# Optimization experiments

Hardware: AMD Instinct MI355X
Metric: run time of the kernel (lower is better)

## Reference

```python
import jax, jax.numpy as jnp
import numpy as np

B, N, D, H = 2, 2048, 1024, 16
DH = D // H
DF = 4 * D
SCALE = D ** (-0.5)  # standard_scale=False -> dim**-0.5
EPS = 1e-5


def _ln(x, w, b):
    mu = jnp.mean(x, axis=-1, keepdims=True)
    var = jnp.mean(jnp.square(x - mu), axis=-1, keepdims=True)
    return (x - mu) * jax.lax.rsqrt(var + EPS) * w + b


def setup_inputs() -> dict:
    key = jax.random.key(0)
    ks = jax.random.split(key, 12)
    s = lambda fan_in: (1.0 / np.sqrt(fan_in))
    return {
        "x": jax.random.normal(ks[0], (B, N, D), jnp.float32),
        "gamma": jax.random.uniform(ks[1], (B, H), jnp.float32),
        "dist_matrix": jax.random.uniform(ks[2], (N, N), jnp.float32),
        "ln1_w": jnp.ones((D,), jnp.float32),
        "ln1_b": jnp.zeros((D,), jnp.float32),
        "qkv_w": jax.random.normal(ks[3], (D, 3 * D), jnp.float32) * s(D),
        "qkv_b": jnp.zeros((3 * D,), jnp.float32),
        "proj_w": jax.random.normal(ks[4], (D, D), jnp.float32) * s(D),
        "proj_b": jnp.zeros((D,), jnp.float32),
        "ln2_w": jnp.ones((D,), jnp.float32),
        "ln2_b": jnp.zeros((D,), jnp.float32),
        "mlp_w1": jax.random.normal(ks[5], (D, DF), jnp.float32) * s(D),
        "mlp_b1": jnp.zeros((DF,), jnp.float32),
        "mlp_w2": jax.random.normal(ks[6], (DF, D), jnp.float32) * s(DF),
        "mlp_b2": jnp.zeros((D,), jnp.float32),
    }


def reference(x, gamma, dist_matrix, ln1_w, ln1_b, qkv_w, qkv_b, proj_w, proj_b,
              ln2_w, ln2_b, mlp_w1, mlp_b1, mlp_w2, mlp_b2):
    # --- ZoomAttention on norm1(x) ---
    h = _ln(x, ln1_w, ln1_b)                                   # [B,N,D]
    qkv = h @ qkv_w + qkv_b                                    # [B,N,3D]
    qkv = qkv.reshape(B, N, 3, H, DH).transpose(2, 0, 3, 1, 4)  # [3,B,H,N,DH]
    q, k, v = qkv[0], qkv[1], qkv[2]
    scores = jnp.einsum("bhnd,bhmd->bhnm", q, k) * SCALE       # [B,H,N,N]
    scores = scores - gamma[:, :, None, None] * dist_matrix[None, None]
    attn = jax.nn.softmax(scores, axis=-1)
    out = jnp.einsum("bhnm,bhmd->bhnd", attn, v)               # [B,H,N,DH]
    out = out.transpose(0, 2, 1, 3).reshape(B, N, D)
    x = x + (out @ proj_w + proj_b)
    # --- MLP (exact GELU, torch default) ---
    h2 = _ln(x, ln2_w, ln2_b)
    h2 = jax.nn.gelu(h2 @ mlp_w1 + mlp_b1, approximate=False) @ mlp_w2 + mlp_b2
    return x + h2
```

## Files before the change

### kernel.cpp

```cpp
#include <hip/hip_runtime.h>
#include <hip/hip_bf16.h>


#define SCALE_ 0.03125f
#define EPS_   1e-5f
#define LOG2E_ 1.4426950408889634f
#define SC2_   (SCALE_ * LOG2E_)

typedef unsigned short u16;
typedef __attribute__((ext_vector_type(8))) short short8;
typedef __attribute__((ext_vector_type(4))) float f32x4;
typedef __attribute__((ext_vector_type(4))) unsigned short u16x4;

__device__ inline float b2f(u16 u){ unsigned x = ((unsigned)u) << 16; float f; __builtin_memcpy(&f, &x, 4); return f; }
__device__ inline u16 f2b(float f){ __hip_bfloat16 h = __float2bfloat16(f); u16 u; __builtin_memcpy(&u, &h, 2); return u; }

__device__ inline void glds16(const u16* g, u16* l) {
    __builtin_amdgcn_global_load_lds(
        (const __attribute__((address_space(1))) void*)g,
        (__attribute__((address_space(3))) void*)l, 16, 0, 0);
}

__device__ inline unsigned cvtpk(float a, float b) {
    unsigned r;
    asm("v_cvt_pk_bf16_f32 %0, %1, %2" : "=v"(r) : "v"(a), "v"(b));
    return r;
}

__global__ __launch_bounds__(256) void prep_fused(
    const float* __restrict__ s0, const float* __restrict__ s1,
    const float* __restrict__ s2, const float* __restrict__ s3,
    u16* __restrict__ d0, u16* __restrict__ d1,
    u16* __restrict__ d2, u16* __restrict__ d3,
    const float* __restrict__ x, const float* __restrict__ lw,
    const float* __restrict__ lb, u16* __restrict__ ho) {
    int bid = blockIdx.x;
    if (bid < 12288) {
        __shared__ float t[32][33];
        const float* src; u16* dst; int K, N, nbx, base;
        if (bid < 3072)      { src = s0; dst = d0; K = 1024; N = 3072; nbx = 96;  base = 0; }
        else if (bid < 4096) { src = s1; dst = d1; K = 1024; N = 1024; nbx = 32;  base = 3072; }
        else if (bid < 8192) { src = s2; dst = d2; K = 1024; N = 4096; nbx = 128; base = 4096; }
        else                 { src = s3; dst = d3; K = 4096; N = 1024; nbx = 32;  base = 8192; }
        int lb2 = bid - base;
        int nb = (lb2 % nbx) * 32, kb = (lb2 / nbx) * 32;
        int tx = threadIdx.x & 31, ty = threadIdx.x >> 5;
        for (int i = 0; i < 4; i++) {
            int r = ty + i * 8;
            t[r][tx] = src[(size_t)(kb + r) * N + nb + tx];
        }
        __syncthreads();
        for (int i = 0; i < 4; i++) {
            int r = ty + i * 8;
            dst[(size_t)(nb + r) * K + kb + tx] = f2b(t[tx][r]);
        }
    } else {
        int row = bid - 12288, t = threadIdx.x;
        float4 v = ((const float4*)(x + (size_t)row * 1024))[t];
        float s1v = v.x + v.y + v.z + v.w;
        float s2v = v.x * v.x + v.y * v.y + v.z * v.z + v.w * v.w;
        for (int o = 32; o > 0; o >>= 1) { s1v += __shfl_xor(s1v, o); s2v += __shfl_xor(s2v, o); }
        __shared__ float a1[4], a2[4];
        if ((t & 63) == 0) { a1[t >> 6] = s1v; a2[t >> 6] = s2v; }
        __syncthreads();
        s1v = a1[0] + a1[1] + a1[2] + a1[3];
        s2v = a2[0] + a2[1] + a2[2] + a2[3];
        float mu = s1v * (1.0f / 1024.0f);
        float var = s2v * (1.0f / 1024.0f) - mu * mu;
        float rs = rsqrtf(var + EPS_);
        float4 wv = ((const float4*)lw)[t];
        float4 bv = ((const float4*)lb)[t];
        u16x4 o;
        o[0] = f2b((v.x - mu) * rs * wv.x + bv.x);
        o[1] = f2b((v.y - mu) * rs * wv.y + bv.y);
        o[2] = f2b((v.z - mu) * rs * wv.z + bv.z);
        o[3] = f2b((v.w - mu) * rs * wv.w + bv.w);
        ((u16x4*)(ho + (size_t)row * 1024))[t] = o;
    }
}

__global__ __launch_bounds__(256) void ln_bf16(const float* __restrict__ x,
                                               const float* __restrict__ w,
                                               const float* __restrict__ b,
                                               u16* __restrict__ out) {
    int row = blockIdx.x, t = threadIdx.x;
    float4 v = ((const float4*)(x + (size_t)row * 1024))[t];
    float s1 = v.x + v.y + v.z + v.w;
    float s2 = v.x * v.x + v.y * v.y + v.z * v.z + v.w * v.w;
    for (int o = 32; o > 0; o >>= 1) { s1 += __shfl_xor(s1, o); s2 += __shfl_xor(s2, o); }
    __shared__ float a1[4], a2[4];
    if ((t & 63) == 0) { a1[t >> 6] = s1; a2[t >> 6] = s2; }
    __syncthreads();
    s1 = a1[0] + a1[1] + a1[2] + a1[3];
    s2 = a2[0] + a2[1] + a2[2] + a2[3];
    float mu = s1 * (1.0f / 1024.0f);
    float var = s2 * (1.0f / 1024.0f) - mu * mu;
    float rs = rsqrtf(var + EPS_);
    float4 wv = ((const float4*)w)[t];
    float4 bv = ((const float4*)b)[t];
    u16x4 o;
    o[0] = f2b((v.x - mu) * rs * wv.x + bv.x);
    o[1] = f2b((v.y - mu) * rs * wv.y + bv.y);
    o[2] = f2b((v.z - mu) * rs * wv.z + bv.z);
    o[3] = f2b((v.w - mu) * rs * wv.w + bv.w);
    ((u16x4*)(out + (size_t)row * 1024))[t] = o;
}

__global__ __launch_bounds__(256) void combine4(
    const u16* __restrict__ p0, const u16* __restrict__ p1,
    const u16* __restrict__ p2, const u16* __restrict__ p3,
    const float* __restrict__ bias, float* __restrict__ out) {
    size_t i = (size_t)(blockIdx.x * 256 + threadIdx.x) * 4;
    u16x4 a0 = *(const u16x4*)(p0 + i);
    u16x4 a1 = *(const u16x4*)(p1 + i);
    u16x4 a2 = *(const u16x4*)(p2 + i);
    u16x4 a3 = *(const u16x4*)(p3 + i);
    float4 ov = *(float4*)(out + i);
    float4 bv = *(const float4*)(bias + (i & 1023));
    ov.x += b2f(a0[0]) + b2f(a1[0]) + b2f(a2[0]) + b2f(a3[0]) + bv.x;
    ov.y += b2f(a0[1]) + b2f(a1[1]) + b2f(a2[1]) + b2f(a3[1]) + bv.y;
    ov.z += b2f(a0[2]) + b2f(a1[2]) + b2f(a2[2]) + b2f(a3[2]) + bv.z;
    ov.w += b2f(a0[3]) + b2f(a1[3]) + b2f(a2[3]) + b2f(a3[3]) + bv.w;
    *(float4*)(out + i) = ov;
}

template <int MODE>
__global__ __launch_bounds__(512) void gemm256_8ph(
    const u16* __restrict__ A, const u16* __restrict__ Bt,
    const float* __restrict__ bias, int K, int ksl,
    u16* __restrict__ outb,
    u16* __restrict__ qp, u16* __restrict__ kp, u16* __restrict__ vtp) {
    __shared__ u16 LS[4][2][256 * 32];
    int tid = threadIdx.x;
    int w = tid >> 6, lane = tid & 63, g = lane >> 4, ln = lane & 15;
    int wr = w >> 2, wc = w & 3;
    int gx = gridDim.x;
    int nwg = gx * gridDim.y;
    int lin = blockIdx.y * gx + blockIdx.x;
    int swz = (lin & 7) * (nwg >> 3) + (lin >> 3);
    int bx = swz % gx, by = swz / gx;
    int br = by * 256, bc = bx * 256;
    int k0 = blockIdx.z * ksl;
    int jx = (((lane & 3) ^ ((lane >> 3) & 3)) << 3);
    const u16* Ast = A + (size_t)(br + w * 32 + (lane >> 2)) * K + k0 + jx;
    const u16* Bst = Bt + (size_t)(bc + w * 32 + (lane >> 2)) * K + k0 + jx;
    size_t r16 = (size_t)16 * K;
    const int ldsW = (w * 32) * 32;
    f32x4 acc[8][4] = {};
    int NT = ksl >> 5;
    int slotr = ((g ^ ((ln >> 1) & 3)) << 3);
    for (int kt = 0; kt < 3; ++kt) {
        glds16(Ast + (size_t)kt * 32, &LS[kt][0][ldsW]);
        glds16(Ast + (size_t)kt * 32 + r16, &LS[kt][0][ldsW + 512]);
        glds16(Bst + (size_t)kt * 32, &LS[kt][1][ldsW]);
        glds16(Bst + (size_t)kt * 32 + r16, &LS[kt][1][ldsW + 512]);
    }
    asm volatile("s_waitcnt vmcnt(8)" ::: "memory");
    __builtin_amdgcn_s_barrier();
    short8 aa[4], bb[4];
    for (int kt = 0; kt < NT; ++kt) {
        const u16* bufA = &LS[kt & 3][0][0];
        const u16* bufB = &LS[kt & 3][1][0];
        int s3 = kt + 3;
        #pragma unroll
        for (int m = 0; m < 4; ++m)
            aa[m] = *(const short8*)&bufA[(wr * 128 + m * 16 + ln) * 32 + slotr];
        #pragma unroll
        for (int n = 0; n < 4; ++n)
            bb[n] = *(const short8*)&bufB[(wc * 64 + n * 16 + ln) * 32 + slotr];
        if (s3 < NT) {
            u16* d = &LS[s3 & 3][0][ldsW];
            glds16(Ast + (size_t)s3 * 32, d);
            glds16(Ast + (size_t)s3 * 32 + r16, d + 512);
        }
        __builtin_amdgcn_s_barrier();
        asm volatile("s_waitcnt lgkmcnt(0)" ::: "memory");
        __builtin_amdgcn_sched_barrier(0);
        __builtin_amdgcn_s_setprio(1);
        #pragma unroll
        for (int m = 0; m < 4; ++m)
            #pragma unroll
            for (int n = 0; n < 4; ++n)
                acc[m][n] = __builtin_amdgcn_mfma_f32_16x16x32_bf16(aa[m], bb[n], acc[m][n], 0, 0, 0);
        __builtin_amdgcn_s_setprio(0);
        __builtin_amdgcn_sched_barrier(0);
        __builtin_amdgcn_s_barrier();
        #pragma unroll
        for (int m = 0; m < 4; ++m)
            aa[m] = *(const short8*)&bufA[(wr * 128 + 64 + m * 16 + ln) * 32 + slotr];
        if (s3 < NT) {
            u16* d = &LS[s3 & 3][1][ldsW];
            glds16(Bst + (size_t)s3 * 32, d);
            glds16(Bst + (size_t)s3 * 32 + r16, d + 512);
        }
        if (kt + 3 < NT)      asm volatile("s_waitcnt vmcnt(8)" ::: "memory");
        else if (kt + 2 < NT) asm volatile("s_waitcnt vmcnt(4)" ::: "memory");
        else if (kt + 1 < NT) asm volatile("s_waitcnt vmcnt(0)" ::: "memory");
        __builtin_amdgcn_s_barrier();
        asm volatile("s_waitcnt lgkmcnt(0)" ::: "memory");
        __builtin_amdgcn_sched_barrier(0);
        __builtin_amdgcn_s_setprio(1);
        #pragma unroll
        for (int m = 0; m < 4; ++m)
            #pragma unroll
            for (int n = 0; n < 4; ++n)
                acc[4 + m][n] = __builtin_amdgcn_mfma_f32_16x16x32_bf16(aa[m], bb[n], acc[4 + m][n], 0, 0, 0);
        __builtin_amdgcn_s_setprio(0);
        __builtin_amdgcn_sched_barrier(0);
        __builtin_amdgcn_s_barrier();
    }
    #pragma unroll
    for (int m = 0; m < 8; ++m) {
        int row0 = br + wr * 128 + m * 16 + g * 4;
        #pragma unroll
        for (int n = 0; n < 4; ++n) {
            int col = bc + wc * 64 + n * 16 + ln;
            if constexpr (MODE == 0) {
                float bv = bias[col];
                int which = col >> 10, cc = col & 1023, hh = cc >> 6, dh = cc & 63;
                int bb2 = row0 >> 11, nn0 = row0 & 2047;
                size_t bh = (size_t)(bb2 * 16 + hh);
                if (which == 0) {
                    for (int r = 0; r < 4; r++)
                        qp[((bh * 2048 + nn0 + r) << 6) + dh] = f2b((acc[m][n][r] + bv) * SC2_);
                } else if (which == 1) {
                    for (int r = 0; r < 4; r++)
                        kp[((bh * 2048 + nn0 + r) << 6) + dh] = f2b(acc[m][n][r] + bv);
                } else {
                    u16x4 o;
                    for (int r = 0; r < 4; r++) o[r] = f2b(acc[m][n][r] + bv);
                    *(u16x4*)&vtp[((bh * 64 + dh) << 11) + nn0] = o;
                }
            } else if constexpr (MODE == 2) {
                float bv = bias[col];
                for (int r = 0; r < 4; r++) {
                    float v = acc[m][n][r] + bv;
                    float gl = 0.5f * v * (1.0f + erff(v * 0.7071067811865476f));
                    outb[(size_t)(row0 + r) * 4096 + col] = f2b(gl);
                }
            } else {
                u16* pb = (blockIdx.z == 0) ? outb : (blockIdx.z == 1) ? qp
                        : (blockIdx.z == 2) ? kp : vtp;
                for (int r = 0; r < 4; r++)
                    pb[(size_t)(row0 + r) * 1024 + col] = f2b(acc[m][n][r]);
            }
        }
    }
}

template <int MODE, int BN>
__global__ __launch_bounds__(256) void gemm_bf16(
    const u16* __restrict__ A, const u16* __restrict__ Bt,
    const float* __restrict__ bias, int M, int N, int K,
    const float* __restrict__ res, float* __restrict__ outf) {
    constexpr int NN = BN / 32;
    __shared__ u16 As[128 * 64];
    __shared__ u16 Bs[BN * 64];
    int br = blockIdx.y * 128, bc = blockIdx.x * BN;
    int tid = threadIdx.x;
    int w = tid >> 6, lane = tid & 63, g = lane >> 4, ln = lane & 15;
    int wr = (w >> 1) * 64, wc = (w & 1) * (BN / 2);
    f32x4 acc[4][NN] = {};
    int sgcol = (((lane & 7) ^ (lane >> 3)) << 3);
    int arow = w * 32 + (lane >> 3);
    int brow = w * (BN / 4) + (lane >> 3);
    const u16* Ap = A + (size_t)(br + arow) * K + sgcol;
    const u16* Bp = Bt + (size_t)(bc + brow) * K + sgcol;
    u16* lA = &As[(w * 32) * 64];
    u16* lB = &Bs[(w * (BN / 4)) * 64];
    size_t rstep = (size_t)8 * K;
    for (int kt = 0; kt < K; kt += 64) {
        __syncthreads();
        #pragma unroll
        for (int i = 0; i < 4; i++) glds16(Ap + kt + i * rstep, lA + i * 512);
        #pragma unroll
        for (int i = 0; i < BN / 32; i++) glds16(Bp + kt + i * rstep, lB + i * 512);
        __syncthreads();
        #pragma unroll
        for (int kk = 0; kk < 2; kk++) {
            int so = (((kk << 2) + g) ^ (ln & 7)) << 3;
            short8 af[4], bfr[NN];
            #pragma unroll
            for (int m = 0; m < 4; m++)  af[m]  = *(const short8*)&As[(wr + m * 16 + ln) * 64 + so];
            #pragma unroll
            for (int n = 0; n < NN; n++) bfr[n] = *(const short8*)&Bs[(wc + n * 16 + ln) * 64 + so];
            #pragma unroll
            for (int m = 0; m < 4; m++)
                #pragma unroll
                for (int n = 0; n < NN; n++)
                    acc[m][n] = __builtin_amdgcn_mfma_f32_16x16x32_bf16(af[m], bfr[n], acc[m][n], 0, 0, 0);
        }
    }
    #pragma unroll
    for (int m = 0; m < 4; m++) {
        int row0 = br + wr + m * 16 + g * 4;
        #pragma unroll
        for (int n = 0; n < NN; n++) {
            int col = bc + wc + n * 16 + ln;
            float bv = bias[col];
            for (int r = 0; r < 4; r++) {
                size_t idx = (size_t)(row0 + r) * 1024 + col;
                outf[idx] = res[idx] + acc[m][n][r] + bv;
            }
        }
    }
}

__global__ __launch_bounds__(512) void attn_fwd(
    const u16* __restrict__ qg, const u16* __restrict__ kg, const u16* __restrict__ vtg,
    const float* __restrict__ dist, const float* __restrict__ gamma, u16* __restrict__ ao) {
    __shared__ u16 Ks[2][64 * 64];
    __shared__ u16 Vs[2][64 * 64];
    __shared__ u16 Ps[8][16 * 64];
    int qt = blockIdx.x, bh = blockIdx.y;
    int b = bh >> 4, h = bh & 15;
    int tid = threadIdx.x, w = tid >> 6, lane = tid & 63, g = lane >> 4, ln = lane & 15;
    float gam = gamma[bh] * LOG2E_;
    int qglob = qt * 128 + w * 16 + ln;
    const u16* qrow = qg + ((size_t)bh * 2048 + qglob) * 64;
    short8 qf0 = *(const short8*)(qrow + g * 8);
    short8 qf1 = *(const short8*)(qrow + 32 + g * 8);
    const float* dbase = dist + (size_t)qglob * 2048 + g * 4;
    float m2 = -3.0e38f, lsum = 0.0f;
    f32x4 acco[4] = {};
    int srow = tid >> 3, seg = tid & 7;
    int ss = ((seg ^ (srow & 7)) << 3);
    const u16* kgp = kg + ((size_t)bh * 2048 + srow) * 64 + seg * 8;
    const u16* vgp = vtg + ((size_t)bh * 64 + srow) * 2048 + seg * 8;
    {
        short8 a0 = *(const short8*)(kgp);
        short8 c0 = *(const short8*)(vgp);
        *(short8*)&Ks[0][srow * 64 + ss] = a0;
        *(short8*)&Vs[0][srow * 64 + ss] = c0;
    }
    f32x4 dcv[4];
    #pragma unroll
    for (int nb = 0; nb < 4; nb++) dcv[nb] = *(const f32x4*)(dbase + nb * 16);
    __syncthreads();
    int cur = 0;
    int so0 = (g ^ (ln & 7)) << 3, so1 = ((4 + g) ^ (ln & 7)) << 3;
    for (int kt = 0; kt < 32; kt++) {
        short8 kr0, vr0;
        f32x4 dnx[4];
        if (kt < 31) {
            kr0 = *(const short8*)(kgp + (kt + 1) * 4096);
            vr0 = *(const short8*)(vgp + (kt + 1) * 64);
            #pragma unroll
            for (int nb = 0; nb < 4; nb++)
                dnx[nb] = *(const f32x4*)(dbase + (kt + 1) * 64 + nb * 16);
        }
        f32x4 sa[4] = {};
        __builtin_amdgcn_s_setprio(1);
        #pragma unroll
        for (int nb = 0; nb < 4; nb++) {
            short8 kf0 = *(const short8*)&Ks[cur][(nb * 16 + ln) * 64 + so0];
            short8 kf1 = *(const short8*)&Ks[cur][(nb * 16 + ln) * 64 + so1];
            sa[nb] = __builtin_amdgcn_mfma_f32_16x16x32_bf16(kf0, qf0, sa[nb], 0, 0, 0);
            sa[nb] = __builtin_amdgcn_mfma_f32_16x16x32_bf16(kf1, qf1, sa[nb], 0, 0, 0);
        }
        __builtin_amdgcn_s_setprio(0);
        float sv[4][4], pm = -3.0e38f;
        #pragma unroll
        for (int nb = 0; nb < 4; nb++) {
            #pragma unroll
            for (int r = 0; r < 4; r++)
                sv[nb][r] = sa[nb][r] - gam * dcv[nb][r];
            pm = fmaxf(pm, fmaxf(fmaxf(sv[nb][0], sv[nb][1]), fmaxf(sv[nb][2], sv[nb][3])));
        }
        pm = fmaxf(pm, __shfl_xor(pm, 16));
        pm = fmaxf(pm, __shfl_xor(pm, 32));
        if (!__all(pm - m2 <= 8.0f)) {
            float nm = fmaxf(m2, pm);
            float al = __builtin_exp2f(m2 - nm);
            m2 = nm;
            lsum *= al;
            #pragma unroll
            for (int db = 0; db < 4; db++) acco[db] *= al;
        }
        #pragma unroll
        for (int nb = 0; nb < 4; nb++) {
            float e0 = __builtin_exp2f(sv[nb][0] - m2);
            float e1 = __builtin_exp2f(sv[nb][1] - m2);
            float e2 = __builtin_exp2f(sv[nb][2] - m2);
            float e3 = __builtin_exp2f(sv[nb][3] - m2);
            lsum += (e0 + e1) + (e2 + e3);
            union { unsigned u[2]; u16x4 v; } pk;
            pk.u[0] = cvtpk(e0, e1);
            pk.u[1] = cvtpk(e2, e3);
            int off = nb * 16 + g * 4;
            *(u16x4*)&Ps[w][ln * 64 + (((off >> 3) ^ (ln & 7)) << 3) + (off & 7)] = pk.v;
        }
        short8 pf0 = *(const short8*)&Ps[w][ln * 64 + so0];
        short8 pf1 = *(const short8*)&Ps[w][ln * 64 + so1];
        __builtin_amdgcn_s_setprio(1);
        #pragma unroll
        for (int db = 0; db < 4; db++) {
            short8 vf0 = *(const short8*)&Vs[cur][(db * 16 + ln) * 64 + so0];
            short8 vf1 = *(const short8*)&Vs[cur][(db * 16 + ln) * 64 + so1];
            acco[db] = __builtin_amdgcn_mfma_f32_16x16x32_bf16(vf0, pf0, acco[db], 0, 0, 0);
            acco[db] = __builtin_amdgcn_mfma_f32_16x16x32_bf16(vf1, pf1, acco[db], 0, 0, 0);
        }
        __builtin_amdgcn_s_setprio(0);
        if (kt < 31) {
            int nx = cur ^ 1;
            *(short8*)&Ks[nx][srow * 64 + ss] = kr0;
            *(short8*)&Vs[nx][srow * 64 + ss] = vr0;
            #pragma unroll
            for (int nb = 0; nb < 4; nb++) dcv[nb] = dnx[nb];
            __syncthreads();
            cur = nx;
        }
    }
    lsum += __shfl_xor(lsum, 16);
    lsum += __shfl_xor(lsum, 32);
    float inv = 1.0f / lsum;
    u16* aop = ao + (size_t)(b * 2048 + qglob) * 1024 + h * 64 + g * 4;
    #pragma unroll
    for (int db = 0; db < 4; db++) {
        u16x4 o;
        #pragma unroll
        for (int r = 0; r < 4; r++) o[r] = f2b(acco[db][r] * inv);
        *(u16x4*)(aop + db * 16) = o;
    }
}

extern "C" void kernel_launch(void* const* d_in, const int* in_sizes, int n_in,
                              void* d_out, int out_size, void* d_ws, size_t ws_size,
                              hipStream_t stream) {
    const float* x     = (const float*)d_in[0];
    const float* gamma = (const float*)d_in[1];
    const float* dist  = (const float*)d_in[2];
    const float* ln1w  = (const float*)d_in[3];
    const float* ln1b  = (const float*)d_in[4];
    const float* qkvw  = (const float*)d_in[5];
    const float* qkvb  = (const float*)d_in[6];
    const float* projw = (const float*)d_in[7];
    const float* projb = (const float*)d_in[8];
    const float* ln2w  = (const float*)d_in[9];
    const float* ln2b  = (const float*)d_in[10];
    const float* w1    = (const float*)d_in[11];
    const float* b1    = (const float*)d_in[12];
    const float* w2    = (const float*)d_in[13];
    const float* b2    = (const float*)d_in[14];
    float* out = (float*)d_out;
    char* ws = (char*)d_ws;
    u16* wqkvT  = (u16*)(ws + 0);
    u16* wprojT = (u16*)(ws + 6291456);
    u16* w1T    = (u16*)(ws + 8388608);
    u16* w2T    = (u16*)(ws + 16777216);
    u16* hb     = (u16*)(ws + 33554432);
    u16* qb     = (u16*)(ws + 41943040);
    u16* kb     = (u16*)(ws + 50331648);
    u16* vtb    = (u16*)(ws + 58720256);
    u16* aob    = (u16*)(ws + 67108864);
    u16* gb     = hb;
    u16* h2b    = aob;
    u16* mp0 = (u16*)(ws + 0);
    u16* mp1 = (u16*)(ws + 8388608);
    u16* mp2 = (u16*)(ws + 25165824);
    u16* mp3 = (u16*)(ws + 67108864);

    dim3 blk(256);
    prep_fused<<<16384, blk, 0, stream>>>(qkvw, projw, w1, w2,
                                          wqkvT, wprojT, w1T, w2T,
                                          x, ln1w, ln1b, hb);
    gemm256_8ph<0><<<dim3(12, 16), dim3(512), 0, stream>>>(hb, wqkvT, qkvb, 1024, 1024,
                                                           nullptr, qb, kb, vtb);
    attn_fwd<<<dim3(16, 32), dim3(512), 0, stream>>>(qb, kb, vtb, dist, gamma, aob);
    gemm_bf16<1, 64><<<dim3(16, 32), blk, 0, stream>>>(aob, wprojT, projb, 4096, 1024, 1024,
                                                       x, out);
    ln_bf16<<<4096, blk, 0, stream>>>(out, ln2w, ln2b, h2b);
    gemm256_8ph<2><<<dim3(16, 16), dim3(512), 0, stream>>>(h2b, w1T, b1, 1024, 1024,
                                                           gb, nullptr, nullptr, nullptr);
    gemm256_8ph<3><<<dim3(4, 16, 4), dim3(512), 0, stream>>>(gb, w2T, nullptr, 4096, 1024,
                                                             mp0, mp1, mp2, mp3);
    combine4<<<4096, blk, 0, stream>>>(mp0, mp1, mp2, mp3, b2, out);
}
```

Before: 254.3 us.

## Split attention over two key halves with a separate log-sum-exp merge kernel

Result: slower. 269.8 us (+6.1%).

```diff
diff --git a/kernel.cpp b/kernel.cpp
--- a/kernel.cpp
+++ b/kernel.cpp
@@ -122,6 +122,32 @@
     ov.z += b2f(a0[2]) + b2f(a1[2]) + b2f(a2[2]) + b2f(a3[2]) + bv.z;
     ov.w += b2f(a0[3]) + b2f(a1[3]) + b2f(a2[3]) + b2f(a3[3]) + bv.w;
     *(float4*)(out + i) = ov;
+}
+
+__global__ __launch_bounds__(256) void attn_merge(
+    const u16* __restrict__ pO0, const u16* __restrict__ pO1,
+    const float2* __restrict__ ml0, const float2* __restrict__ ml1,
+    u16* __restrict__ ao) {
+    int t = blockIdx.x * 256 + threadIdx.x;
+    int bh = t >> 11, q = t & 2047;
+    int b = bh >> 4, h = bh & 15;
+    float2 s0 = ml0[t], s1 = ml1[t];
+    float M = fmaxf(s0.x, s1.x);
+    float e0 = __builtin_exp2f(s0.x - M);
+    float e1 = __builtin_exp2f(s1.x - M);
+    float inv = 1.0f / (e0 * s0.y + e1 * s1.y);
+    float c0 = e0 * inv, c1 = e1 * inv;
+    const u16x4* r0 = (const u16x4*)(pO0 + (size_t)t * 64);
+    const u16x4* r1 = (const u16x4*)(pO1 + (size_t)t * 64);
+    u16* aop = ao + ((size_t)(b * 2048 + q)) * 1024 + h * 64;
+    #pragma unroll
+    for (int i = 0; i < 16; ++i) {
+        u16x4 a = r0[i], c = r1[i], o;
+        #pragma unroll
+        for (int j = 0; j < 4; ++j)
+            o[j] = f2b(b2f(a[j]) * c0 + b2f(c[j]) * c1);
+        *(u16x4*)(aop + i * 4) = o;
+    }
 }
 
 template <int MODE>
@@ -308,25 +334,26 @@
 
 __global__ __launch_bounds__(512) void attn_fwd(
     const u16* __restrict__ qg, const u16* __restrict__ kg, const u16* __restrict__ vtg,
-    const float* __restrict__ dist, const float* __restrict__ gamma, u16* __restrict__ ao) {
+    const float* __restrict__ dist, const float* __restrict__ gamma,
+    u16* __restrict__ pO0, u16* __restrict__ pO1,
+    float2* __restrict__ ml0, float2* __restrict__ ml1) {
     __shared__ u16 Ks[2][64 * 64];
     __shared__ u16 Vs[2][64 * 64];
     __shared__ u16 Ps[8][16 * 64];
-    int qt = blockIdx.x, bh = blockIdx.y;
-    int b = bh >> 4, h = bh & 15;
+    int qt = blockIdx.x, bh = blockIdx.y, z = blockIdx.z;
     int tid = threadIdx.x, w = tid >> 6, lane = tid & 63, g = lane >> 4, ln = lane & 15;
     float gam = gamma[bh] * LOG2E_;
     int qglob = qt * 128 + w * 16 + ln;
     const u16* qrow = qg + ((size_t)bh * 2048 + qglob) * 64;
     short8 qf0 = *(const short8*)(qrow + g * 8);
     short8 qf1 = *(const short8*)(qrow + 32 + g * 8);
-    const float* dbase = dist + (size_t)qglob * 2048 + g * 4;
+    const float* dbase = dist + (size_t)qglob * 2048 + z * 1024 + g * 4;
     float m2 = -3.0e38f, lsum = 0.0f;
     f32x4 acco[4] = {};
     int srow = tid >> 3, seg = tid & 7;
     int ss = ((seg ^ (srow & 7)) << 3);
-    const u16* kgp = kg + ((size_t)bh * 2048 + srow) * 64 + seg * 8;
-    const u16* vgp = vtg + ((size_t)bh * 64 + srow) * 2048 + seg * 8;
+    const u16* kgp = kg + ((size_t)(bh * 2048 + z * 1024 + srow)) * 64 + seg * 8;
+    const u16* vgp = vtg + ((size_t)(bh * 64 + srow)) * 2048 + z * 1024 + seg * 8;
     {
         short8 a0 = *(const short8*)(kgp);
         short8 c0 = *(const short8*)(vgp);
@@ -339,10 +366,10 @@
     __syncthreads();
     int cur = 0;
     int so0 = (g ^ (ln & 7)) << 3, so1 = ((4 + g) ^ (ln & 7)) << 3;
-    for (int kt = 0; kt < 32; kt++) {
+    for (int kt = 0; kt < 16; kt++) {
         short8 kr0, vr0;
         f32x4 dnx[4];
-        if (kt < 31) {
+        if (kt < 15) {
             kr0 = *(const short8*)(kgp + (kt + 1) * 4096);
             vr0 = *(const short8*)(vgp + (kt + 1) * 64);
             #pragma unroll
@@ -401,7 +428,7 @@
             acco[db] = __builtin_amdgcn_mfma_f32_16x16x32_bf16(vf1, pf1, acco[db], 0, 0, 0);
         }
         __builtin_amdgcn_s_setprio(0);
-        if (kt < 31) {
+        if (kt < 15) {
             int nx = cur ^ 1;
             *(short8*)&Ks[nx][srow * 64 + ss] = kr0;
             *(short8*)&Vs[nx][srow * 64 + ss] = vr0;
@@ -413,14 +440,18 @@
     }
     lsum += __shfl_xor(lsum, 16);
     lsum += __shfl_xor(lsum, 32);
-    float inv = 1.0f / lsum;
-    u16* aop = ao + (size_t)(b * 2048 + qglob) * 1024 + h * 64 + g * 4;
+    int rowid = (bh << 11) + qglob;
+    u16* po = (z ? pO1 : pO0) + (size_t)rowid * 64 + g * 4;
     #pragma unroll
     for (int db = 0; db < 4; db++) {
         u16x4 o;
         #pragma unroll
-        for (int r = 0; r < 4; r++) o[r] = f2b(acco[db][r] * inv);
-        *(u16x4*)(aop + db * 16) = o;
+        for (int r = 0; r < 4; r++) o[r] = f2b(acco[db][r]);
+        *(u16x4*)(po + db * 16) = o;
+    }
+    if (g == 0) {
+        float2 s; s.x = m2; s.y = lsum;
+        (z ? ml1 : ml0)[rowid] = s;
     }
 }
 
@@ -455,6 +486,10 @@
     u16* aob    = (u16*)(ws + 67108864);
     u16* gb     = hb;
     u16* h2b    = aob;
+    u16*    pO0 = (u16*)(ws + 25165824);
+    u16*    pO1 = (u16*)(ws + 33554432);
+    float2* ml0 = (float2*)(ws + 0);
+    float2* ml1 = (float2*)(ws + 1048576);
     u16* mp0 = (u16*)(ws + 0);
     u16* mp1 = (u16*)(ws + 8388608);
     u16* mp2 = (u16*)(ws + 25165824);
@@ -466,7 +501,9 @@
                                           x, ln1w, ln1b, hb);
     gemm256_8ph<0><<<dim3(12, 16), dim3(512), 0, stream>>>(hb, wqkvT, qkvb, 1024, 1024,
                                                            nullptr, qb, kb, vtb);
-    attn_fwd<<<dim3(16, 32), dim3(512), 0, stream>>>(qb, kb, vtb, dist, gamma, aob);
+    attn_fwd<<<dim3(16, 32, 2), dim3(512), 0, stream>>>(qb, kb, vtb, dist, gamma,
+                                                        pO0, pO1, ml0, ml1);
+    attn_merge<<<256, blk, 0, stream>>>(pO0, pO1, ml0, ml1, aob);
     gemm_bf16<1, 64><<<dim3(16, 32), blk, 0, stream>>>(aob, wprojT, projb, 4096, 1024, 1024,
                                                        x, out);
     ln_bf16<<<4096, blk, 0, stream>>>(out, ln2w, ln2b, h2b);
```

## Software-pipeline attention: compute next tile's QK scores during current softmax

Applied to the files above, without the earlier changes.

Measured after the change: 271.4 us. +6.7%, slower.

```diff
diff --git a/kernel.cpp b/kernel.cpp
--- a/kernel.cpp
+++ b/kernel.cpp
@@ -309,8 +309,8 @@
 __global__ __launch_bounds__(512) void attn_fwd(
     const u16* __restrict__ qg, const u16* __restrict__ kg, const u16* __restrict__ vtg,
     const float* __restrict__ dist, const float* __restrict__ gamma, u16* __restrict__ ao) {
-    __shared__ u16 Ks[2][64 * 64];
-    __shared__ u16 Vs[2][64 * 64];
+    __shared__ u16 Ks[4][64 * 64];
+    __shared__ u16 Vs[4][64 * 64];
     __shared__ u16 Ps[8][16 * 64];
     int qt = blockIdx.x, bh = blockIdx.y;
     int b = bh >> 4, h = bh & 15;
@@ -330,87 +330,116 @@
     {
         short8 a0 = *(const short8*)(kgp);
         short8 c0 = *(const short8*)(vgp);
+        short8 a1 = *(const short8*)(kgp + 4096);
+        short8 c1 = *(const short8*)(vgp + 64);
         *(short8*)&Ks[0][srow * 64 + ss] = a0;
         *(short8*)&Vs[0][srow * 64 + ss] = c0;
+        *(short8*)&Ks[1][srow * 64 + ss] = a1;
+        *(short8*)&Vs[1][srow * 64 + ss] = c1;
     }
     f32x4 dcv[4];
     #pragma unroll
     for (int nb = 0; nb < 4; nb++) dcv[nb] = *(const f32x4*)(dbase + nb * 16);
     __syncthreads();
-    int cur = 0;
     int so0 = (g ^ (ln & 7)) << 3, so1 = ((4 + g) ^ (ln & 7)) << 3;
-    for (int kt = 0; kt < 32; kt++) {
-        short8 kr0, vr0;
-        f32x4 dnx[4];
-        if (kt < 31) {
-            kr0 = *(const short8*)(kgp + (kt + 1) * 4096);
-            vr0 = *(const short8*)(vgp + (kt + 1) * 64);
-            #pragma unroll
-            for (int nb = 0; nb < 4; nb++)
-                dnx[nb] = *(const f32x4*)(dbase + (kt + 1) * 64 + nb * 16);
-        }
-        f32x4 sa[4] = {};
+    f32x4 saA[4] = {}, saB[4] = {};
+    {
         __builtin_amdgcn_s_setprio(1);
         #pragma unroll
         for (int nb = 0; nb < 4; nb++) {
-            short8 kf0 = *(const short8*)&Ks[cur][(nb * 16 + ln) * 64 + so0];
-            short8 kf1 = *(const short8*)&Ks[cur][(nb * 16 + ln) * 64 + so1];
-            sa[nb] = __builtin_amdgcn_mfma_f32_16x16x32_bf16(kf0, qf0, sa[nb], 0, 0, 0);
-            sa[nb] = __builtin_amdgcn_mfma_f32_16x16x32_bf16(kf1, qf1, sa[nb], 0, 0, 0);
+            short8 kf0 = *(const short8*)&Ks[0][(nb * 16 + ln) * 64 + so0];
+            short8 kf1 = *(const short8*)&Ks[0][(nb * 16 + ln) * 64 + so1];
+            saA[nb] = __builtin_amdgcn_mfma_f32_16x16x32_bf16(kf0, qf0, saA[nb], 0, 0, 0);
+            saA[nb] = __builtin_amdgcn_mfma_f32_16x16x32_bf16(kf1, qf1, saA[nb], 0, 0, 0);
         }
         __builtin_amdgcn_s_setprio(0);
-        float sv[4][4], pm = -3.0e38f;
-        #pragma unroll
-        for (int nb = 0; nb < 4; nb++) {
-            #pragma unroll
-            for (int r = 0; r < 4; r++)
-                sv[nb][r] = sa[nb][r] - gam * dcv[nb][r];
-            pm = fmaxf(pm, fmaxf(fmaxf(sv[nb][0], sv[nb][1]), fmaxf(sv[nb][2], sv[nb][3])));
-        }
-        pm = fmaxf(pm, __shfl_xor(pm, 16));
-        pm = fmaxf(pm, __shfl_xor(pm, 32));
-        if (!__all(pm - m2 <= 8.0f)) {
-            float nm = fmaxf(m2, pm);
-            float al = __builtin_exp2f(m2 - nm);
-            m2 = nm;
-            lsum *= al;
-            #pragma unroll
-            for (int db = 0; db < 4; db++) acco[db] *= al;
-        }
-        #pragma unroll
-        for (int nb = 0; nb < 4; nb++) {
-            float e0 = __builtin_exp2f(sv[nb][0] - m2);
-            float e1 = __builtin_exp2f(sv[nb][1] - m2);
-            float e2 = __builtin_exp2f(sv[nb][2] - m2);
-            float e3 = __builtin_exp2f(sv[nb][3] - m2);
-            lsum += (e0 + e1) + (e2 + e3);
-            union { unsigned u[2]; u16x4 v; } pk;
-            pk.u[0] = cvtpk(e0, e1);
-            pk.u[1] = cvtpk(e2, e3);
-            int off = nb * 16 + g * 4;
-            *(u16x4*)&Ps[w][ln * 64 + (((off >> 3) ^ (ln & 7)) << 3) + (off & 7)] = pk.v;
-        }
-        short8 pf0 = *(const short8*)&Ps[w][ln * 64 + so0];
-        short8 pf1 = *(const short8*)&Ps[w][ln * 64 + so1];
-        __builtin_amdgcn_s_setprio(1);
-        #pragma unroll
-        for (int db = 0; db < 4; db++) {
-            short8 vf0 = *(const short8*)&Vs[cur][(db * 16 + ln) * 64 + so0];
-            short8 vf1 = *(const short8*)&Vs[cur][(db * 16 + ln) * 64 + so1];
-            acco[db] = __builtin_amdgcn_mfma_f32_16x16x32_bf16(vf0, pf0, acco[db], 0, 0, 0);
-            acco[db] = __builtin_amdgcn_mfma_f32_16x16x32_bf16(vf1, pf1, acco[db], 0, 0, 0);
-        }
-        __builtin_amdgcn_s_setprio(0);
-        if (kt < 31) {
-            int nx = cur ^ 1;
-            *(short8*)&Ks[nx][srow * 64 + ss] = kr0;
-            *(short8*)&Vs[nx][srow * 64 + ss] = vr0;
-            #pragma unroll
-            for (int nb = 0; nb < 4; nb++) dcv[nb] = dnx[nb];
-            __syncthreads();
-            cur = nx;
-        }
-    }
+    }
+
+#define ATTN_STEP(SA_CUR, SA_NXT, T)                                                     \
+    {                                                                                    \
+        short8 kr0, vr0;                                                                 \
+        f32x4 dnx[4];                                                                    \
+        if ((T) < 30) {                                                                  \
+            kr0 = *(const short8*)(kgp + ((T) + 2) * 4096);                              \
+            vr0 = *(const short8*)(vgp + ((T) + 2) * 64);                                \
+        }                                                                                \
+        if ((T) < 31) {                                                                  \
+            _Pragma("unroll")                                                            \
+            for (int nb = 0; nb < 4; nb++)                                               \
+                dnx[nb] = *(const f32x4*)(dbase + ((T) + 1) * 64 + nb * 16);             \
+            const u16* KB = &Ks[((T) + 1) & 3][0];                                       \
+            __builtin_amdgcn_s_setprio(1);                                               \
+            _Pragma("unroll")                                                            \
+            for (int nb = 0; nb < 4; nb++) {                                             \
+                short8 kf0 = *(const short8*)&KB[(nb * 16 + ln) * 64 + so0];             \
+                short8 kf1 = *(const short8*)&KB[(nb * 16 + ln) * 64 + so1];             \
+                f32x4 t0 = {};                                                           \
+                t0 = __builtin_amdgcn_mfma_f32_16x16x32_bf16(kf0, qf0, t0, 0, 0, 0);     \
+                SA_NXT[nb] = __builtin_amdgcn_mfma_f32_16x16x32_bf16(kf1, qf1, t0, 0, 0, 0); \
+            }                                                                            \
+            __builtin_amdgcn_s_setprio(0);                                               \
+        }                                                                                \
+        float sv[4][4], pm = -3.0e38f;                                                   \
+        _Pragma("unroll")                                                                \
+        for (int nb = 0; nb < 4; nb++) {                                                 \
+            _Pragma("unroll")                                                            \
+            for (int r = 0; r < 4; r++)                                                  \
+                sv[nb][r] = SA_CUR[nb][r] - gam * dcv[nb][r];                            \
+            pm = fmaxf(pm, fmaxf(fmaxf(sv[nb][0], sv[nb][1]), fmaxf(sv[nb][2], sv[nb][3]))); \
+        }                                                                                \
+        pm = fmaxf(pm, __shfl_xor(pm, 16));                                              \
+        pm = fmaxf(pm, __shfl_xor(pm, 32));                                              \
+        if (!__all(pm - m2 <= 8.0f)) {                                                   \
+            float nm = fmaxf(m2, pm);                                                    \
+            float al = __builtin_exp2f(m2 - nm);                                         \
+            m2 = nm;                                                                     \
+            lsum *= al;                                                                  \
+            _Pragma("unroll")                                                            \
+            for (int db = 0; db < 4; db++) acco[db] *= al;                               \
+        }                                                                                \
+        _Pragma("unroll")                                                                \
+        for (int nb = 0; nb < 4; nb++) {                                                 \
+            float e0 = __builtin_exp2f(sv[nb][0] - m2);                                  \
+            float e1 = __builtin_exp2f(sv[nb][1] - m2);                                  \
+            float e2 = __builtin_exp2f(sv[nb][2] - m2);                                  \
+            float e3 = __builtin_exp2f(sv[nb][3] - m2);                                  \
+            lsum += (e0 + e1) + (e2 + e3);                                               \
+            union { unsigned u[2]; u16x4 v; } pk;                                        \
+            pk.u[0] = cvtpk(e0, e1);                                                     \
+            pk.u[1] = cvtpk(e2, e3);                                                     \
+            int off = nb * 16 + g * 4;                                                   \
+            *(u16x4*)&Ps[w][ln * 64 + (((off >> 3) ^ (ln & 7)) << 3) + (off & 7)] = pk.v; \
+        }                                                                                \
+        short8 pf0 = *(const short8*)&Ps[w][ln * 64 + so0];                              \
+        short8 pf1 = *(const short8*)&Ps[w][ln * 64 + so1];                              \
+        const u16* VB = &Vs[(T) & 3][0];                                                 \
+        __builtin_amdgcn_s_setprio(1);                                                   \
+        _Pragma("unroll")                                                                \
+        for (int db = 0; db < 4; db++) {                                                 \
+            short8 vf0 = *(const short8*)&VB[(db * 16 + ln) * 64 + so0];                 \
+            short8 vf1 = *(const short8*)&VB[(db * 16 + ln) * 64 + so1];                 \
+            acco[db] = __builtin_amdgcn_mfma_f32_16x16x32_bf16(vf0, pf0, acco[db], 0, 0, 0); \
+            acco[db] = __builtin_amdgcn_mfma_f32_16x16x32_bf16(vf1, pf1, acco[db], 0, 0, 0); \
+        }                                                                                \
+        __builtin_amdgcn_s_setprio(0);                                                   \
+        if ((T) < 30) {                                                                  \
+            *(short8*)&Ks[((T) + 2) & 3][srow * 64 + ss] = kr0;                          \
+            *(short8*)&Vs[((T) + 2) & 3][srow * 64 + ss] = vr0;                          \
+        }                                                                                \
+        if ((T) < 31) {                                                                  \
+            _Pragma("unroll")                                                            \
+            for (int nb = 0; nb < 4; nb++) dcv[nb] = dnx[nb];                            \
+            __syncthreads();                                                             \
+        }                                                                                \
+    }
+
+    #pragma unroll
+    for (int t2 = 0; t2 < 32; t2 += 2) {
+        ATTN_STEP(saA, saB, t2);
+        ATTN_STEP(saB, saA, t2 + 1);
+    }
+#undef ATTN_STEP
+
     lsum += __shfl_xor(lsum, 16);
     lsum += __shfl_xor(lsum, 32);
     float inv = 1.0f / lsum;
```
